# Kernel optimization log

Hardware: AMD Instinct MI355X
Metric: run time of the kernel (lower is better)

Reference implementation:

```python
import jax, jax.numpy as jnp
import numpy as np

D = 128        # embed_dims
P = 4          # num_points
G = 1          # num_groups
L = 4          # num_levels
NC = 6         # cameras
HB, WB = 200, 200
QN = HB * WB
NUM_LAYERS = 2
IMG_H, IMG_W = 256, 704
EPS = 1e-5
PC_MIN = np.array([-50.0, -50.0, -5.0], np.float32)
PC_EXT = np.array([100.0, 100.0, 8.0], np.float32)
LEVEL_HW = [(32, 88), (16, 44), (8, 22), (4, 11)]


def layer_norm(x, g, b):
    m = x.mean(-1, keepdims=True)
    v = jnp.mean((x - m) ** 2, axis=-1, keepdims=True)
    return (x - m) * jax.lax.rsqrt(v + 1e-5) * g + b


def bilinear(feat, u, v):
    # feat: (B,H,W,C); u,v: (B,N) normalized to [0,1]; zero padding, align_corners=False
    B, H, W, C = feat.shape
    x = u * W - 0.5
    y = v * H - 0.5
    x0f = jnp.floor(x)
    y0f = jnp.floor(y)
    wx = (x - x0f)[..., None]
    wy = (y - y0f)[..., None]
    x0 = x0f.astype(jnp.int32)
    y0 = y0f.astype(jnp.int32)
    bi = jnp.arange(B)[:, None]

    def gather(xi, yi):
        valid = ((xi >= 0) & (xi < W) & (yi >= 0) & (yi < H)).astype(feat.dtype)[..., None]
        return feat[bi, jnp.clip(yi, 0, H - 1), jnp.clip(xi, 0, W - 1)] * valid

    return (gather(x0, y0) * (1 - wx) * (1 - wy)
            + gather(x0 + 1, y0) * wx * (1 - wy)
            + gather(x0, y0 + 1) * (1 - wx) * wy
            + gather(x0 + 1, y0 + 1) * wx * wy)


def cam_contrib(l2i_n, hom, sw, cam_feats):
    # l2i_n: (B,4,4); hom: (B,Q,G,P,4); sw: (B,Q,G,P,L); cam_feats: L x (B,Hl,Wl,C)
    p2 = jnp.einsum('bij,bqgpj->bqgpi', l2i_n, hom)
    z = p2[..., 2]
    zc = jnp.maximum(z, EPS)
    u = p2[..., 0] / (zc * IMG_W)
    v = p2[..., 1] / (zc * IMG_H)
    mask = (z > EPS) & (u >= 0) & (u <= 1) & (v >= 0) & (v <= 1)
    B = hom.shape[0]
    uf = u.reshape(B, -1)
    vf = v.reshape(B, -1)
    out = jnp.zeros(hom.shape[:4] + (cam_feats[0].shape[-1],), cam_feats[0].dtype)
    for l in range(L):
        s = bilinear(cam_feats[l], uf, vf).reshape(B, -1, G, P, cam_feats[l].shape[-1])
        out = out + s * sw[..., l:l + 1]
    return out * mask[..., None].astype(out.dtype)


def forward(feat0, feat1, feat2, feat3, lidar2img, bev_query, bev_pos,
            pe_w1, pe_b1, pe_w2, pe_b2, conv1_w, conv1_b, conv2_w, conv2_b,
            off_w, off_b, sw_w, sw_b, cp_w1, cp_b1, cp_w2, cp_b2, cp_w3, cp_b3,
            ffn_w1, ffn_b1, ffn_w2, ffn_b2, n1_g, n1_b, n2_g, n2_b, n3_g, n3_b):
    # (b,n,C,h,w) -> (b,n,h,w,C), matching the decoder's rearrange (g=1)
    feats = [jnp.transpose(f, (0, 1, 3, 4, 2)) for f in (feat0, feat1, feat2, feat3)]
    B = bev_query.shape[0]
    pc_min = jnp.asarray(PC_MIN)
    pc_ext = jnp.asarray(PC_EXT)
    # position embedding of bev_pos is identical every layer
    pos_embed = jax.nn.relu(bev_pos @ pe_w1 + pe_b1) @ pe_w2 + pe_b2
    q = bev_query
    for _ in range(NUM_LAYERS):
        # in_conv: 1x1 conv + GELU + 5x5 conv on 200x200 BEV grid
        qe = (q + pos_embed).reshape(B, HB, WB, D)
        h = jax.nn.gelu(qe @ conv1_w + conv1_b, approximate=False)
        h = jax.lax.conv_general_dilated(h, conv2_w, (1, 1), 'SAME',
                                         dimension_numbers=('NHWC', 'HWIO', 'NHWC')) + conv2_b
        q = q + h.reshape(B, QN, D)
        q = layer_norm(q, n1_g, n1_b)
        # DetSegSampling
        off = (q @ off_w + off_b).reshape(B, QN, G, P, 3)
        ref = bev_pos[:, :, None, None, :] * pc_ext + pc_min
        pts = ref + off
        sw = jax.nn.softmax((q @ sw_w + sw_b).reshape(B, QN, G, P, L), axis=-1)
        hom = jnp.concatenate([pts, jnp.ones_like(pts[..., :1])], -1)
        acc = jnp.zeros((B, QN, G, P, D), q.dtype)
        for n in range(NC):
            acc = acc + cam_contrib(lidar2img[:, n], hom, sw,
                                    tuple(f[:, n] for f in feats))
        # 'b q g p c -> b q (p g c)' then 3-layer compressor MLP (1x1 convs)
        flat = jnp.transpose(acc, (0, 1, 3, 2, 4)).reshape(B, QN, P * G * D)
        h = jax.nn.relu(flat @ cp_w1 + cp_b1)
        h = jax.nn.relu(h @ cp_w2 + cp_b2)
        h = h @ cp_w3 + cp_b3
        q = q + h
        q = layer_norm(q, n2_g, n2_b)
        q = q + (jax.nn.relu(q @ ffn_w1 + ffn_b1) @ ffn_w2 + ffn_b2)
        q = layer_norm(q, n3_g, n3_b)
    return q


def _make_lidar2img():
    fx = fy = 500.0
    K = np.array([[fx, 0, IMG_W / 2, 0], [0, fy, IMG_H / 2, 0],
                  [0, 0, 1, 0], [0, 0, 0, 1]], np.float32)
    mats = []
    for n in range(NC):
        yaw = 2 * np.pi * n / NC
        c, s = np.cos(yaw), np.sin(yaw)
        # camera n looks along (cos yaw, sin yaw, 0), mounted 1.5m above lidar
        E = np.array([[s, -c, 0, 0], [0, 0, -1, 1.5], [c, s, 0, 0], [0, 0, 0, 1]], np.float32)
        mats.append(K @ E)
    return jnp.asarray(np.stack(mats))[None]  # (1,NC,4,4)


def setup_inputs() -> dict:
    key = jax.random.key(0)
    ks = jax.random.split(key, 24)
    sc = 0.02
    inp = {}
    for i, (h, w) in enumerate(LEVEL_HW):
        inp[f'feat{i}'] = jax.random.normal(ks[i], (1, NC, D, h, w), jnp.float32)
    inp['lidar2img'] = _make_lidar2img()
    inp['bev_query'] = jax.random.normal(ks[4], (1, QN, D), jnp.float32)
    inp['bev_pos'] = jax.random.uniform(ks[5], (1, QN, 3), jnp.float32)
    inp['pe_w1'] = jax.random.normal(ks[6], (3, 2 * D), jnp.float32) * sc
    inp['pe_b1'] = jnp.zeros((2 * D,), jnp.float32)
    inp['pe_w2'] = jax.random.normal(ks[7], (2 * D, D), jnp.float32) * sc
    inp['pe_b2'] = jnp.zeros((D,), jnp.float32)
    inp['conv1_w'] = jax.random.normal(ks[8], (D, D), jnp.float32) * sc
    inp['conv1_b'] = jnp.zeros((D,), jnp.float32)
    inp['conv2_w'] = jax.random.normal(ks[9], (5, 5, D, D), jnp.float32) * sc
    inp['conv2_b'] = jnp.zeros((D,), jnp.float32)
    inp['off_w'] = jax.random.normal(ks[10], (D, G * P * 3), jnp.float32) * 0.01
    inp['off_b'] = jax.random.uniform(ks[11], (G * P * 3,), jnp.float32, -0.5, 0.5)
    inp['sw_w'] = jax.random.normal(ks[12], (D, G * P * L), jnp.float32) * sc
    inp['sw_b'] = jnp.zeros((G * P * L,), jnp.float32)
    inp['cp_w1'] = jax.random.normal(ks[13], (P * G * D, 4 * D), jnp.float32) * sc
    inp['cp_b1'] = jnp.zeros((4 * D,), jnp.float32)
    inp['cp_w2'] = jax.random.normal(ks[14], (4 * D, 4 * D), jnp.float32) * sc
    inp['cp_b2'] = jnp.zeros((4 * D,), jnp.float32)
    inp['cp_w3'] = jax.random.normal(ks[15], (4 * D, D), jnp.float32) * sc
    inp['cp_b3'] = jnp.zeros((D,), jnp.float32)
    inp['ffn_w1'] = jax.random.normal(ks[16], (D, D), jnp.float32) * sc
    inp['ffn_b1'] = jnp.zeros((D,), jnp.float32)
    inp['ffn_w2'] = jax.random.normal(ks[17], (D, D), jnp.float32) * sc
    inp['ffn_b2'] = jnp.zeros((D,), jnp.float32)
    for i in (1, 2, 3):
        inp[f'n{i}_g'] = jnp.ones((D,), jnp.float32)
        inp[f'n{i}_b'] = jnp.zeros((D,), jnp.float32)
    return inp


def reference(feat0, feat1, feat2, feat3, lidar2img, bev_query, bev_pos,
              pe_w1, pe_b1, pe_w2, pe_b2, conv1_w, conv1_b, conv2_w, conv2_b,
              off_w, off_b, sw_w, sw_b, cp_w1, cp_b1, cp_w2, cp_b2, cp_w3, cp_b3,
              ffn_w1, ffn_b1, ffn_w2, ffn_b2, n1_g, n1_b, n2_g, n2_b, n3_g, n3_b):
    return forward(feat0, feat1, feat2, feat3, lidar2img, bev_query, bev_pos,
                   pe_w1, pe_b1, pe_w2, pe_b2, conv1_w, conv1_b, conv2_w, conv2_b,
                   off_w, off_b, sw_w, sw_b, cp_w1, cp_b1, cp_w2, cp_b2, cp_w3, cp_b3,
                   ffn_w1, ffn_b1, ffn_w2, ffn_b2, n1_g, n1_b, n2_g, n2_b, n3_g, n3_b)
```

## Files before the change

kernel.cpp:

```cpp
#include <hip/hip_runtime.h>
#include <hip/hip_bf16.h>

typedef unsigned short u16;
typedef unsigned char u8;
typedef __attribute__((ext_vector_type(8))) short bf16x8;
typedef __attribute__((ext_vector_type(4))) float f32x4;
typedef __attribute__((ext_vector_type(2))) float f32x2;

#define DEV __device__ __forceinline__

DEV float b2f(u16 s){ return __uint_as_float(((unsigned)s) << 16); }
DEV u16 f2b(float f){
    unsigned u = __float_as_uint(f);
    u = u + 0x7fffu + ((u >> 16) & 1u);
    return (u16)(u >> 16);
}
DEV u8 f2f8(float v){
    int r = __builtin_amdgcn_cvt_pk_fp8_f32(v, v, 0, false);
    return (u8)(r & 0xff);
}
DEV unsigned f2f8x4(float a, float b, float c, float d){
    int lo = __builtin_amdgcn_cvt_pk_fp8_f32(a, b, 0, false);
    int r  = __builtin_amdgcn_cvt_pk_fp8_f32(c, d, lo, true);
    return (unsigned)r;
}
DEV void storeElem(float* p, float v){ *p = v; }
DEV void storeElem(u16* p, float v){ *p = f2b(v); }
DEV void storeElem(u8* p, float v){ *p = f2f8(v); }

template<int ACT> DEV float actf(float x){
    if (ACT == 1) return fmaxf(x, 0.f);
    if (ACT == 2) return 0.5f * x * (1.f + erff(x * 0.70710678118654752f));
    return x;
}

DEV void gload16(const void* g, void* l){
    __builtin_amdgcn_global_load_lds(
        (const __attribute__((address_space(1))) void*)g,
        (__attribute__((address_space(3))) void*)l, 16, 0, 0);
}

__global__ void transpose_feat(const float* __restrict__ in, u8* __restrict__ out,
                               int H, int W){
    int total = 6 * H * W * 32;
    int lin = blockIdx.x * 256 + threadIdx.x;
    if (lin >= total) return;
    int c4   = (lin & 31) * 4;
    int pix  = lin >> 5;
    int x    = pix % W;
    int rest = pix / W;
    int y    = rest % H;
    int n    = rest / H;
    int HW   = H * W;
    size_t ib = ((size_t)(n * 128 + c4) * H + y) * W + x;
    unsigned v4 = f2f8x4(in[ib], in[ib + (size_t)HW],
                         in[ib + (size_t)2 * HW], in[ib + (size_t)3 * HW]);
    *(unsigned*)&out[(size_t)pix * 128 + c4] = v4;
}

__global__ void prep_wt(const float* __restrict__ w, u16* __restrict__ o, int K, int N){
    int id = blockIdx.x * 256 + threadIdx.x;
    if (id >= K * N) return;
    int n = id / K, k = id % K;
    o[id] = f2b(w[(size_t)k * N + n]);
}
__global__ void prep_wt_f8(const float* __restrict__ w, u8* __restrict__ o, int K, int N){
    int id = blockIdx.x * 256 + threadIdx.x;
    if (id >= K * N) return;
    int n = id / K, k = id % K;
    o[id] = f2f8(w[(size_t)k * N + n]);
}
__global__ void prep_osw_w(const float* __restrict__ off_w, const float* __restrict__ off_b,
                           const float* __restrict__ sw_w, const float* __restrict__ sw_b,
                           u16* __restrict__ owsT, float* __restrict__ obias){
    int id = blockIdx.x * 256 + threadIdx.x;
    if (id >= 4096) return;
    int n = id >> 7, k = id & 127;
    float w = (n < 12) ? off_w[k * 12 + n] : (n < 28) ? sw_w[k * 16 + (n - 12)] : 0.f;
    owsT[n * 128 + k] = f2b(w);
    if (k == 0) obias[n] = (n < 12) ? off_b[n] : (n < 28) ? sw_b[n - 12] : 0.f;
}
__global__ void prep_conv_w_f8(const float* __restrict__ w, u8* __restrict__ o){
    int id = blockIdx.x * 256 + threadIdx.x;
    if (id >= 51200) return;
    int slot = id & 15;
    int oc   = (id >> 4) & 127;
    int tap  = id >> 11;
    int ks = slot >> 2, kg = slot & 3;
    int ic0 = ks * 32 + kg * 8;
    u8 tmp[8];
#pragma unroll
    for (int j = 0; j < 8; j++)
        tmp[j] = f2f8(w[((size_t)tap * 128 + ic0 + j) * 128 + oc]);
    *(long*)&o[(size_t)tap * 16384 + ks * 4096 + kg * 1024 + oc * 8] = *(long*)tmp;
}
__global__ void prep_hid(const float* __restrict__ bev_pos,
                         const float* __restrict__ w1, const float* __restrict__ b1,
                         u16* __restrict__ hid){
    int id = blockIdx.x * 256 + threadIdx.x;
    if (id >= 2560000) return;
    int qi = id >> 6, c4 = (id & 63) * 4;
    float p0 = bev_pos[qi * 3 + 0];
    float p1 = bev_pos[qi * 3 + 1];
    float p2 = bev_pos[qi * 3 + 2];
    ushort4 v;
    u16* vp = (u16*)&v;
#pragma unroll
    for (int j = 0; j < 4; j++){
        int ch = c4 + j;
        float h = p0 * w1[ch] + p1 * w1[256 + ch] + p2 * w1[512 + ch] + b1[ch];
        vp[j] = f2b(fmaxf(h, 0.f));
    }
    *(ushort4*)&hid[(size_t)qi * 256 + c4] = v;
}

DEV void stage64(const u16* __restrict__ g, int ldk, u16* lds, int wv, int lane){
    const u16* gp = g + (size_t)(lane >> 3) * ldk + (lane & 7) * 8;
#pragma unroll
    for (int j = 0; j < 4; j++){
        int ch = wv + j * 4;
        gload16(gp + (size_t)ch * 8 * ldk, lds + ch * 512);
    }
}
DEV void stage64f8(const u8* __restrict__ g, int ldk, u8* lds, int wv, int lane){
    int rloc = lane >> 2;
#pragma unroll
    for (int j = 0; j < 2; j++){
        int ch = wv + j * 4;
        int row = ch * 16 + rloc;
        int sp  = (lane & 3) ^ ((row >> 1) & 3);
        gload16(g + (size_t)row * ldk + sp * 16, lds + ch * 1024);
    }
}

template<int K, int ACT, typename TOUT, int NBY = 0, int NBX = 0>
__global__ __launch_bounds__(256) void mfma_gemm(
    const u16* __restrict__ A, const u16* __restrict__ BT,
    const float* __restrict__ bias, TOUT* __restrict__ C, int Ntot){
    __shared__ u16 As[2][128 * 64];
    __shared__ u16 Bs[2][128 * 64];
    const int t = threadIdx.x, wv = t >> 6, lane = t & 63;
    int bx, by;
    if (NBY > 0){
        const int gpx = (NBX + 7) / 8;
        int xcd = blockIdx.x & 7, slot = blockIdx.x >> 3;
        bx = xcd * gpx + slot / NBY;
        by = slot % NBY;
        if (bx >= NBX) return;
    } else { bx = blockIdx.x; by = blockIdx.y; }
    const int r0 = bx * 128, n0 = by * 128;
    const int l15 = lane & 15, kg = lane >> 4;
    const int wr = (wv >> 1) * 64, wc = (wv & 1) * 64;
    f32x4 acc[4][4];
#pragma unroll
    for (int r = 0; r < 4; r++)
#pragma unroll
        for (int c = 0; c < 4; c++) acc[r][c] = (f32x4){0.f, 0.f, 0.f, 0.f};

    stage64(A + (size_t)r0 * K, K, As[0], wv, lane);
    stage64(BT + (size_t)n0 * K, K, Bs[0], wv, lane);
    __syncthreads();
    int buf = 0;
    for (int kc = 0; kc < K / 64; kc++){
        if (kc + 1 < K / 64){
            stage64(A + (size_t)r0 * K + (kc + 1) * 64, K, As[buf ^ 1], wv, lane);
            stage64(BT + (size_t)n0 * K + (kc + 1) * 64, K, Bs[buf ^ 1], wv, lane);
        }
#pragma unroll
        for (int ks = 0; ks < 2; ks++){
            bf16x8 af[4], bfr[4];
#pragma unroll
            for (int r = 0; r < 4; r++)
                af[r] = *(const bf16x8*)&As[buf][(wr + r * 16 + l15) * 64 + ks * 32 + kg * 8];
#pragma unroll
            for (int c = 0; c < 4; c++)
                bfr[c] = *(const bf16x8*)&Bs[buf][(wc + c * 16 + l15) * 64 + ks * 32 + kg * 8];
#pragma unroll
            for (int r = 0; r < 4; r++)
#pragma unroll
                for (int c = 0; c < 4; c++)
                    acc[r][c] = __builtin_amdgcn_mfma_f32_16x16x32_bf16(af[r], bfr[c], acc[r][c], 0, 0, 0);
        }
        __syncthreads();
        buf ^= 1;
    }
#pragma unroll
    for (int c = 0; c < 4; c++){
        int gcol = n0 + wc + c * 16 + l15;
        float bb = bias[gcol];
#pragma unroll
        for (int r = 0; r < 4; r++){
#pragma unroll
            for (int reg = 0; reg < 4; reg++){
                int grow = r0 + wr + r * 16 + kg * 4 + reg;
                storeElem(C + (size_t)grow * Ntot + gcol, actf<ACT>(acc[r][c][reg] + bb));
            }
        }
    }
}

template<int K, int ACT, typename TOUT, int NBY = 0, int NBX = 0>
__global__ __launch_bounds__(256) void mfma_gemm_f8(
    const u8* __restrict__ A, const u8* __restrict__ BT,
    const float* __restrict__ bias, TOUT* __restrict__ C, int Ntot){
    __shared__ __align__(16) u8 As[2][128 * 64];
    __shared__ __align__(16) u8 Bs[2][128 * 64];
    const int t = threadIdx.x, wv = t >> 6, lane = t & 63;
    int bx, by;
    if (NBY > 0){
        const int gpx = (NBX + 7) / 8;
        int xcd = blockIdx.x & 7, slot = blockIdx.x >> 3;
        bx = xcd * gpx + slot / NBY;
        by = slot % NBY;
        if (bx >= NBX) return;
    } else { bx = blockIdx.x; by = blockIdx.y; }
    const int r0 = bx * 128, n0 = by * 128;
    const int l15 = lane & 15, kg = lane >> 4;
    const int wr = (wv >> 1) * 64, wc = (wv & 1) * 64;
    f32x4 acc[4][4];
#pragma unroll
    for (int r = 0; r < 4; r++)
#pragma unroll
        for (int c = 0; c < 4; c++) acc[r][c] = (f32x4){0.f, 0.f, 0.f, 0.f};

    stage64f8(A + (size_t)r0 * K, K, As[0], wv, lane);
    stage64f8(BT + (size_t)n0 * K, K, Bs[0], wv, lane);
    __syncthreads();
    int buf = 0;
    for (int kc = 0; kc < K / 64; kc++){
        if (kc + 1 < K / 64){
            stage64f8(A + (size_t)r0 * K + (kc + 1) * 64, K, As[buf ^ 1], wv, lane);
            stage64f8(BT + (size_t)n0 * K + (kc + 1) * 64, K, Bs[buf ^ 1], wv, lane);
        }
#pragma unroll
        for (int ks = 0; ks < 2; ks++){
            long af[4], bfr[4];
#pragma unroll
            for (int r = 0; r < 4; r++){
                int row = wr + r * 16 + l15;
                int s8 = (ks * 4 + kg) ^ (row & 6);
                af[r] = *(const long*)&As[buf][row * 64 + s8 * 8];
            }
#pragma unroll
            for (int c = 0; c < 4; c++){
                int row = wc + c * 16 + l15;
                int s8 = (ks * 4 + kg) ^ (row & 6);
                bfr[c] = *(const long*)&Bs[buf][row * 64 + s8 * 8];
            }
#pragma unroll
            for (int r = 0; r < 4; r++)
#pragma unroll
                for (int c = 0; c < 4; c++)
                    acc[r][c] = __builtin_amdgcn_mfma_f32_16x16x32_fp8_fp8(af[r], bfr[c], acc[r][c], 0, 0, 0);
        }
        __syncthreads();
        buf ^= 1;
    }
#pragma unroll
    for (int c = 0; c < 4; c++){
        int gcol = n0 + wc + c * 16 + l15;
        float bb = bias[gcol];
#pragma unroll
        for (int r = 0; r < 4; r++){
#pragma unroll
            for (int reg = 0; reg < 4; reg++){
                int grow = r0 + wr + r * 16 + kg * 4 + reg;
                storeElem(C + (size_t)grow * Ntot + gcol, actf<ACT>(acc[r][c][reg] + bb));
            }
        }
    }
}

__global__ __launch_bounds__(256) void mfma_pos(
    const u16* __restrict__ A, const u16* __restrict__ BT,
    const float* __restrict__ bias, const float* __restrict__ bq,
    float* __restrict__ pos, u16* __restrict__ qp16){
    const int K = 256;
    __shared__ u16 As[2][128 * 64];
    __shared__ u16 Bs[2][128 * 64];
    const int t = threadIdx.x, wv = t >> 6, lane = t & 63;
    const int r0 = blockIdx.x * 128;
    const int l15 = lane & 15, kg = lane >> 4;
    const int wr = (wv >> 1) * 64, wc = (wv & 1) * 64;
    f32x4 acc[4][4];
#pragma unroll
    for (int r = 0; r < 4; r++)
#pragma unroll
        for (int c = 0; c < 4; c++) acc[r][c] = (f32x4){0.f, 0.f, 0.f, 0.f};

    stage64(A + (size_t)r0 * K, K, As[0], wv, lane);
    stage64(BT, K, Bs[0], wv, lane);
    __syncthreads();
    int buf = 0;
    for (int kc = 0; kc < 4; kc++){
        if (kc + 1 < 4){
            stage64(A + (size_t)r0 * K + (kc + 1) * 64, K, As[buf ^ 1], wv, lane);
            stage64(BT + (kc + 1) * 64, K, Bs[buf ^ 1], wv, lane);
        }
#pragma unroll
        for (int ks = 0; ks < 2; ks++){
            bf16x8 af[4], bfr[4];
#pragma unroll
            for (int r = 0; r < 4; r++)
                af[r] = *(const bf16x8*)&As[buf][(wr + r * 16 + l15) * 64 + ks * 32 + kg * 8];
#pragma unroll
            for (int c = 0; c < 4; c++)
                bfr[c] = *(const bf16x8*)&Bs[buf][(wc + c * 16 + l15) * 64 + ks * 32 + kg * 8];
#pragma unroll
            for (int r = 0; r < 4; r++)
#pragma unroll
                for (int c = 0; c < 4; c++)
                    acc[r][c] = __builtin_amdgcn_mfma_f32_16x16x32_bf16(af[r], bfr[c], acc[r][c], 0, 0, 0);
        }
        __syncthreads();
        buf ^= 1;
    }
#pragma unroll
    for (int c = 0; c < 4; c++){
        int gcol = wc + c * 16 + l15;
        float bb = bias[gcol];
#pragma unroll
        for (int r = 0; r < 4; r++){
#pragma unroll
            for (int reg = 0; reg < 4; reg++){
                int grow = r0 + wr + r * 16 + kg * 4 + reg;
                int growc = min(grow, 39999);
                float v = acc[r][c][reg] + bb;
                pos[(size_t)grow * 128 + gcol]  = v;
                qp16[(size_t)grow * 128 + gcol] = f2b(v + bq[(size_t)growc * 128 + gcol]);
            }
        }
    }
}

template<int AUXM>
__global__ __launch_bounds__(256) void mfma_ffn_ln(
    const u16* __restrict__ A, const u16* __restrict__ W1T,
    const float* __restrict__ b1, const u16* __restrict__ W2T,
    const float* __restrict__ b2, const float* __restrict__ qin,
    const float* __restrict__ gam, const float* __restrict__ bet,
    float* __restrict__ outf, u16* __restrict__ aux,
    const float* __restrict__ pos, int Mlim){
    __shared__ u16 As[2][128 * 64];
    __shared__ u16 Bs[2][128 * 64];
    const int t = threadIdx.x, wv = t >> 6, lane = t & 63;
    const int r0 = blockIdx.x * 128;
    const int l15 = lane & 15, kg = lane >> 4;
    const int wr = wv * 32;
    f32x4 acc[2][8];
#pragma unroll
    for (int r = 0; r < 2; r++)
#pragma unroll
        for (int c = 0; c < 8; c++) acc[r][c] = (f32x4){0.f, 0.f, 0.f, 0.f};

    stage64(A + (size_t)r0 * 128, 128, As[0], wv, lane);
    stage64(A + (size_t)r0 * 128 + 64, 128, As[1], wv, lane);
    stage64(W1T, 128, Bs[0], wv, lane);
    stage64(W1T + 64, 128, Bs[1], wv, lane);
    __syncthreads();
#pragma unroll
    for (int kc = 0; kc < 2; kc++){
#pragma unroll
        for (int ks = 0; ks < 2; ks++){
            bf16x8 af[2], bfr[8];
#pragma unroll
            for (int r = 0; r < 2; r++)
                af[r] = *(const bf16x8*)&As[kc][(wr + r * 16 + l15) * 64 + ks * 32 + kg * 8];
#pragma unroll
            for (int c = 0; c < 8; c++)
                bfr[c] = *(const bf16x8*)&Bs[kc][(c * 16 + l15) * 64 + ks * 32 + kg * 8];
#pragma unroll
            for (int r = 0; r < 2; r++)
#pragma unroll
                for (int c = 0; c < 8; c++)
                    acc[r][c] = __builtin_amdgcn_mfma_f32_16x16x32_bf16(af[r], bfr[c], acc[r][c], 0, 0, 0);
        }
    }
    __syncthreads();
    stage64(W2T, 128, Bs[0], wv, lane);
    stage64(W2T + 64, 128, Bs[1], wv, lane);
#pragma unroll
    for (int c = 0; c < 8; c++){
        int col = c * 16 + l15;
        float bb1 = b1[col];
#pragma unroll
        for (int r = 0; r < 2; r++)
#pragma unroll
            for (int reg = 0; reg < 4; reg++){
                int rowl = wr + r * 16 + kg * 4 + reg;
                As[col >> 6][rowl * 64 + (col & 63)] = f2b(fmaxf(acc[r][c][reg] + bb1, 0.f));
            }
    }
    __syncthreads();
#pragma unroll
    for (int r = 0; r < 2; r++)
#pragma unroll
        for (int c = 0; c < 8; c++) acc[r][c] = (f32x4){0.f, 0.f, 0.f, 0.f};
#pragma unroll
    for (int kc = 0; kc < 2; kc++){
#pragma unroll
        for (int ks = 0; ks < 2; ks++){
            bf16x8 af[2], bfr[8];
#pragma unroll
            for (int r = 0; r < 2; r++)
                af[r] = *(const bf16x8*)&As[kc][(wr + r * 16 + l15) * 64 + ks * 32 + kg * 8];
#pragma unroll
            for (int c = 0; c < 8; c++)
                bfr[c] = *(const bf16x8*)&Bs[kc][(c * 16 + l15) * 64 + ks * 32 + kg * 8];
#pragma unroll
            for (int r = 0; r < 2; r++)
#pragma unroll
                for (int c = 0; c < 8; c++)
                    acc[r][c] = __builtin_amdgcn_mfma_f32_16x16x32_bf16(af[r], bfr[c], acc[r][c], 0, 0, 0);
        }
    }
    float bb[8], gg[8], be[8];
#pragma unroll
    for (int c = 0; c < 8; c++){
        int col = c * 16 + l15;
        bb[c] = b2[col]; gg[c] = gam[col]; be[c] = bet[col];
    }
#pragma unroll
    for (int r = 0; r < 2; r++){
#pragma unroll
        for (int reg = 0; reg < 4; reg++){
            int grow = r0 + wr + r * 16 + kg * 4 + reg;
            const float* qrow = qin + (size_t)grow * 128;
            float s = 0.f, q2 = 0.f;
#pragma unroll
            for (int c = 0; c < 8; c++){
                float x = acc[r][c][reg] + bb[c] + qrow[c * 16 + l15];
                acc[r][c][reg] = x;
                s += x; q2 += x * x;
            }
#pragma unroll
            for (int m = 8; m >= 1; m >>= 1){
                s  += __shfl_xor(s, m, 64);
                q2 += __shfl_xor(q2, m, 64);
            }
            float mean = s * 0.0078125f;
            float var  = q2 * 0.0078125f - mean * mean;
            float rs   = rsqrtf(var + 1e-5f);
            bool wr_ok = grow < Mlim;
#pragma unroll
            for (int c = 0; c < 8; c++){
                float o = (acc[r][c][reg] - mean) * rs * gg[c] + be[c];
                int col = c * 16 + l15;
                if (wr_ok){
                    outf[(size_t)grow * 128 + col] = o;
                    if (AUXM == 2)
                        aux[(size_t)grow * 128 + col] = f2b(o + pos[(size_t)grow * 128 + col]);
                }
            }
        }
    }
}

template<int K, int AUXM>
__global__ __launch_bounds__(256) void mfma_gemm_ln_f8(
    const u8* __restrict__ A, const u8* __restrict__ BT,
    const float* __restrict__ bias, const float* __restrict__ qin,
    const float* __restrict__ gam, const float* __restrict__ bet,
    float* __restrict__ outf, u16* __restrict__ aux,
    const float* __restrict__ pos, int Mlim){
    __shared__ __align__(16) u8 As[2][128 * 64];
    __shared__ __align__(16) u8 Bs[2][128 * 64];
    const int t = threadIdx.x, wv = t >> 6, lane = t & 63;
    const int r0 = blockIdx.x * 128;
    const int l15 = lane & 15, kg = lane >> 4;
    const int wr = wv * 32;
    f32x4 acc[2][8];
#pragma unroll
    for (int r = 0; r < 2; r++)
#pragma unroll
        for (int c = 0; c < 8; c++) acc[r][c] = (f32x4){0.f, 0.f, 0.f, 0.f};

    stage64f8(A + (size_t)r0 * K, K, As[0], wv, lane);
    stage64f8(BT, K, Bs[0], wv, lane);
    __syncthreads();
    int buf = 0;
    for (int kc = 0; kc < K / 64; kc++){
        if (kc + 1 < K / 64){
            stage64f8(A + (size_t)r0 * K + (kc + 1) * 64, K, As[buf ^ 1], wv, lane);
            stage64f8(BT + (kc + 1) * 64, K, Bs[buf ^ 1], wv, lane);
        }
#pragma unroll
        for (int ks = 0; ks < 2; ks++){
            long af[2], bfr[8];
#pragma unroll
            for (int r = 0; r < 2; r++){
                int row = wr + r * 16 + l15;
                int s8 = (ks * 4 + kg) ^ (row & 6);
                af[r] = *(const long*)&As[buf][row * 64 + s8 * 8];
            }
#pragma unroll
            for (int c = 0; c < 8; c++){
                int row = c * 16 + l15;
                int s8 = (ks * 4 + kg) ^ (row & 6);
                bfr[c] = *(const long*)&Bs[buf][row * 64 + s8 * 8];
            }
#pragma unroll
            for (int r = 0; r < 2; r++)
#pragma unroll
                for (int c = 0; c < 8; c++)
                    acc[r][c] = __builtin_amdgcn_mfma_f32_16x16x32_fp8_fp8(af[r], bfr[c], acc[r][c], 0, 0, 0);
        }
        __syncthreads();
        buf ^= 1;
    }
    float bb[8], gg[8], be[8];
#pragma unroll
    for (int c = 0; c < 8; c++){
        int col = c * 16 + l15;
        bb[c] = bias[col]; gg[c] = gam[col]; be[c] = bet[col];
    }
#pragma unroll
    for (int r = 0; r < 2; r++){
#pragma unroll
        for (int reg = 0; reg < 4; reg++){
            int grow = r0 + wr + r * 16 + kg * 4 + reg;
            const float* qrow = qin + (size_t)grow * 128;
            float s = 0.f, q2 = 0.f;
#pragma unroll
            for (int c = 0; c < 8; c++){
                float x = acc[r][c][reg] + bb[c] + qrow[c * 16 + l15];
                acc[r][c][reg] = x;
                s += x; q2 += x * x;
            }
#pragma unroll
            for (int m = 8; m >= 1; m >>= 1){
                s  += __shfl_xor(s, m, 64);
                q2 += __shfl_xor(q2, m, 64);
            }
            float mean = s * 0.0078125f;
            float var  = q2 * 0.0078125f - mean * mean;
            float rs   = rsqrtf(var + 1e-5f);
            bool wr_ok = grow < Mlim;
#pragma unroll
            for (int c = 0; c < 8; c++){
                float o = (acc[r][c][reg] - mean) * rs * gg[c] + be[c];
                int col = c * 16 + l15;
                if (wr_ok){
                    outf[(size_t)grow * 128 + col] = o;
                    if (AUXM == 1) aux[(size_t)grow * 128 + col] = f2b(o);
                    else if (AUXM == 2)
                        aux[(size_t)grow * 128 + col] = f2b(o + pos[(size_t)grow * 128 + col]);
                }
            }
        }
    }
}

__global__ __launch_bounds__(256) void mfma_osw(
    const u16* __restrict__ A, const u16* __restrict__ BT,
    const float* __restrict__ bias, float* __restrict__ osw){
    __shared__ u16 As[2][128 * 64];
    __shared__ u16 Bs[2][32 * 64];
    const int t = threadIdx.x, wv = t >> 6, lane = t & 63;
    const int r0 = blockIdx.x * 128;
    const int l15 = lane & 15, kg = lane >> 4;
#pragma unroll
    for (int it = 0; it < 8; it++){
        int id = it * 256 + t;
        int row = id >> 4, slot = id & 15;
        uint4 v = *(const uint4*)&A[(size_t)(r0 + row) * 128 + slot * 8];
        *(uint4*)&As[slot >> 3][row * 64 + (slot & 7) * 8] = v;
    }
#pragma unroll
    for (int it = 0; it < 2; it++){
        int id = it * 256 + t;
        if (id < 512){
            int row = id >> 4, slot = id & 15;
            uint4 v = *(const uint4*)&BT[(size_t)row * 128 + slot * 8];
            *(uint4*)&Bs[slot >> 3][row * 64 + (slot & 7) * 8] = v;
        }
    }
    __syncthreads();
    f32x4 acc[2][2];
#pragma unroll
    for (int r = 0; r < 2; r++)
#pragma unroll
        for (int c = 0; c < 2; c++) acc[r][c] = (f32x4){0.f, 0.f, 0.f, 0.f};
#pragma unroll
    for (int ks = 0; ks < 4; ks++){
        int h = ks >> 1, koff = (ks & 1) * 32 + kg * 8;
        bf16x8 af[2], bfr[2];
#pragma unroll
        for (int r = 0; r < 2; r++)
            af[r] = *(const bf16x8*)&As[h][(wv * 32 + r * 16 + l15) * 64 + koff];
#pragma unroll
        for (int c = 0; c < 2; c++)
            bfr[c] = *(const bf16x8*)&Bs[h][(c * 16 + l15) * 64 + koff];
#pragma unroll
        for (int r = 0; r < 2; r++)
#pragma unroll
            for (int c = 0; c < 2; c++)
                acc[r][c] = __builtin_amdgcn_mfma_f32_16x16x32_bf16(af[r], bfr[c], acc[r][c], 0, 0, 0);
    }
#pragma unroll
    for (int c = 0; c < 2; c++){
        int gcol = c * 16 + l15;
        float bb = bias[gcol];
#pragma unroll
        for (int r = 0; r < 2; r++)
#pragma unroll
            for (int reg = 0; reg < 4; reg++){
                int grow = r0 + wv * 32 + r * 16 + kg * 4 + reg;
                osw[(size_t)grow * 32 + gcol] = acc[r][c][reg] + bb;
            }
    }
}

__global__ __launch_bounds__(256) void proj_kernel(
    const float* __restrict__ osw, const float* __restrict__ bev_pos,
    const float* __restrict__ l2i, float* __restrict__ ent, int* __restrict__ cntb){
    int id = blockIdx.x * 256 + threadIdx.x;
    int qi = id >> 2, p = id & 3;
    const float* row = osw + (size_t)qi * 32;
    float px = bev_pos[qi * 3 + 0] * 100.f - 50.f + row[p * 3 + 0];
    float py = bev_pos[qi * 3 + 1] * 100.f - 50.f + row[p * 3 + 1];
    float pz = bev_pos[qi * 3 + 2] * 8.f   - 5.f  + row[p * 3 + 2];
    float lg[4];
#pragma unroll
    for (int l = 0; l < 4; l++) lg[l] = row[12 + p * 4 + l];
    float mx = fmaxf(fmaxf(lg[0], lg[1]), fmaxf(lg[2], lg[3]));
    float den = 0.f, sw[4];
#pragma unroll
    for (int l = 0; l < 4; l++){ sw[l] = expf(lg[l] - mx); den += sw[l]; }
    float inv = 1.f / den;
#pragma unroll
    for (int l = 0; l < 4; l++) sw[l] *= inv;

    const int HS[4] = {32, 16, 8, 4};
    const int WS[4] = {88, 44, 22, 11};
    const unsigned LOFF[4] = {0u, 2162688u, 2703360u, 2838528u};
    int cnt = 0;
    for (int cam = 0; cam < 6; cam++){
        const float* M = l2i + cam * 16;
        float t0 = M[0] * px + M[1] * py + M[2]  * pz + M[3];
        float t1 = M[4] * px + M[5] * py + M[6]  * pz + M[7];
        float z  = M[8] * px + M[9] * py + M[10] * pz + M[11];
        float zc = fmaxf(z, 1e-5f);
        float u = t0 / (zc * 704.f);
        float v = t1 / (zc * 256.f);
        if (!((z > 1e-5f) && u >= 0.f && u <= 1.f && v >= 0.f && v <= 1.f)) continue;
#pragma unroll
        for (int l = 0; l < 4; l++){
            const int Hl = HS[l], Wl = WS[l];
            float xx = u * (float)Wl - 0.5f;
            float yy = v * (float)Hl - 0.5f;
            float xf = floorf(xx), yf = floorf(yy);
            float wx = xx - xf, wy = yy - yf;
            int ix = (int)xf, iy = (int)yf;
            float sl = sw[l];
            float wx0 = (ix >= 0)      ? 1.f - wx : 0.f;
            float wx1 = (ix < Wl - 1)  ? wx       : 0.f;
            float wy0 = (iy >= 0)      ? 1.f - wy : 0.f;
            float wy1 = (iy < Hl - 1)  ? wy       : 0.f;
            int x0c = max(ix, 0), x1c = min(ix + 1, Wl - 1);
            int y0c = max(iy, 0), y1c = min(iy + 1, Hl - 1);
            unsigned base = LOFF[l] + (unsigned)cam * (unsigned)(Hl * Wl * 128)
                          + (unsigned)(y0c * Wl + x0c) * 128u;
            unsigned dxdy = (unsigned)((x1c - x0c) * 128)
                          | ((unsigned)((y1c - y0c) * Wl * 128) << 16);
            if (cnt < 8){
                float* ep = ent + ((size_t)cnt * 160000 + id) * 8;
                float4 w4;
                w4.x = sl * wx0 * wy0; w4.y = sl * wx1 * wy0;
                w4.z = sl * wx0 * wy1; w4.w = sl * wx1 * wy1;
                *(float4*)ep = w4;
                float4 m4;
                m4.x = __uint_as_float(base); m4.y = __uint_as_float(dxdy);
                m4.z = 0.f; m4.w = 0.f;
                *(float4*)(ep + 4) = m4;
                cnt++;
            }
        }
    }
    cntb[id] = cnt;
}

DEV void fma8f8(float* acc, uint2 v, float w){
    f32x2 p0 = __builtin_amdgcn_cvt_pk_f32_fp8(v.x, false);
    f32x2 p1 = __builtin_amdgcn_cvt_pk_f32_fp8(v.x, true);
    f32x2 p2 = __builtin_amdgcn_cvt_pk_f32_fp8(v.y, false);
    f32x2 p3 = __builtin_amdgcn_cvt_pk_f32_fp8(v.y, true);
    acc[0] = fmaf(p0.x, w, acc[0]);
    acc[1] = fmaf(p0.y, w, acc[1]);
    acc[2] = fmaf(p1.x, w, acc[2]);
    acc[3] = fmaf(p1.y, w, acc[3]);
    acc[4] = fmaf(p2.x, w, acc[4]);
    acc[5] = fmaf(p2.y, w, acc[5]);
    acc[6] = fmaf(p3.x, w, acc[6]);
    acc[7] = fmaf(p3.y, w, acc[7]);
}

__global__ __launch_bounds__(256) void sample_kernel(
    const float* __restrict__ ent, const int* __restrict__ cntb,
    const u8* __restrict__ ftbase, u8* __restrict__ flat){
    const int t = threadIdx.x;
    const int lane = t & 15;
    const int id = blockIdx.x * 16 + (t >> 4);
    const int d0 = lane * 8;
    const int cnt = cntb[id];
    float acc[8] = {0, 0, 0, 0, 0, 0, 0, 0};

    float4 wA, wB; float2 mA, mB;
    if (cnt > 0){
        const float* ep = ent + ((size_t)id) * 8;
        wA = *(const float4*)ep;
        mA = *(const float2*)(ep + 4);
    }
    for (int e = 0; e < cnt; e++){
        if (e + 1 < cnt){
            const float* ep = ent + ((size_t)(e + 1) * 160000 + id) * 8;
            wB = *(const float4*)ep;
            mB = *(const float2*)(ep + 4);
        }
        unsigned base = __float_as_uint(mA.x) + (unsigned)d0;
        unsigned dxdy = __float_as_uint(mA.y);
        unsigned dx = dxdy & 0xffffu, dy = dxdy >> 16;
        uint2 v00 = *(const uint2*)(ftbase + base);
        uint2 v10 = *(const uint2*)(ftbase + base + dx);
        uint2 v01 = *(const uint2*)(ftbase + base + dy);
        uint2 v11 = *(const uint2*)(ftbase + base + dx + dy);
        fma8f8(acc, v00, wA.x);
        fma8f8(acc, v10, wA.y);
        fma8f8(acc, v01, wA.z);
        fma8f8(acc, v11, wA.w);
        wA = wB; mA = mB;
    }
    uint2 o;
    o.x = f2f8x4(acc[0], acc[1], acc[2], acc[3]);
    o.y = f2f8x4(acc[4], acc[5], acc[6], acc[7]);
    *(uint2*)&flat[(size_t)id * 128 + d0] = o;
}

#define ALOAD(S, DST) if ((S) < 100){                                                 \
    const int tap_ = (S) >> 2, ks_ = (S) & 3;                                         \
    const int ky_ = tap_ / 5, kx_ = tap_ - ky_ * 5;                                   \
    const int s8_ = ks_ * 4 + kg;                                                     \
    _Pragma("unroll")                                                                 \
    for (int fb = 0; fb < 2; fb++){                                                   \
        _Pragma("unroll")                                                             \
        for (int fp = 0; fp < 2; fp++){                                               \
            int pr_ = fb * 4 + (l15 >> 2) + ky_;                                      \
            int pc_ = fp * 4 + (l15 & 3) + kx_;                                       \
            int pix_ = pr_ * 12 + pc_;                                                \
            int sw_ = ((s8_ >> 1) ^ (pc_ + 4 * pr_)) & 7;                             \
            DST[fb * 2 + fp] = *(const long*)((const char*)Ps + pix_ * 128            \
                                              + sw_ * 16 + (s8_ & 1) * 8);            \
        }                                                                             \
    }                                                                                 \
}
#define CMFMA(CURA, CURB) {                                                           \
    _Pragma("unroll")                                                                 \
    for (int fr = 0; fr < 4; fr++){                                                   \
        acc[fr][0] = __builtin_amdgcn_mfma_f32_16x16x32_fp8_fp8(CURA[fr], CURB[0], acc[fr][0], 0, 0, 0); \
        acc[fr][1] = __builtin_amdgcn_mfma_f32_16x16x32_fp8_fp8(CURA[fr], CURB[1], acc[fr][1], 0, 0, 0); \
    }                                                                                 \
}
#define LOADB(S, DST) if ((S) < 100){                                                 \
    const u8* wp_ = wfrag + ((S) >> 2) * 16384 + ((S) & 3) * 4096                     \
                   + kg * 1024 + (wc + l15) * 8;                                      \
    DST[0] = *(const long*)(wp_);                                                     \
    DST[1] = *(const long*)(wp_ + 128);                                               \
}

__global__ __launch_bounds__(256, 4) void conv5_ln(
    const u8* __restrict__ in,
    const u8* __restrict__ wfrag,
    const float* __restrict__ bias,
    const float* __restrict__ qin,
    const float* __restrict__ gam, const float* __restrict__ bet,
    float* __restrict__ qb, u16* __restrict__ q16){
    __shared__ __align__(16) u8 Ps[144 * 128];
    const int t = threadIdx.x, wv = t >> 6, lane = t & 63;
    const int bx = blockIdx.x % 25, by = blockIdx.x / 25;
    const int x0 = bx * 8, y0 = by * 8;
    const int l15 = lane & 15, kg = lane >> 4;
    const int wc = wv * 32;

#pragma unroll
    for (int it = 0; it < 5; it++){
        int id = it * 256 + t;
        if (id < 1152){
            int pix = id >> 3, slot = id & 7;
            int pr = pix / 12, pc = pix - pr * 12;
            int gy = y0 + pr - 2, gx = x0 + pc - 2;
            uint4 v = {0u, 0u, 0u, 0u};
            if (gy >= 0 && gy < 200 && gx >= 0 && gx < 200)
                v = *(const uint4*)&in[(size_t)(gy * 200 + gx) * 128 + slot * 16];
            int s = (slot ^ (pc + 4 * pr)) & 7;
            *(uint4*)((char*)Ps + pix * 128 + s * 16) = v;
        }
    }
    f32x4 acc[4][2];
#pragma unroll
    for (int r = 0; r < 4; r++){
        acc[r][0] = (f32x4){0.f, 0.f, 0.f, 0.f};
        acc[r][1] = (f32x4){0.f, 0.f, 0.f, 0.f};
    }

    long b0[2], b1[2], b2[2], b3[2];
    LOADB(0, b0); LOADB(1, b1); LOADB(2, b2);
    __syncthreads();

    long aA[4], aB[4];
    ALOAD(0, aA);

    for (int i = 0; i < 25; i++){
        int s = i * 4;
        LOADB(s + 3, b3); ALOAD(s + 1, aB); CMFMA(aA, b0);
        LOADB(s + 4, b0); ALOAD(s + 2, aA); CMFMA(aB, b1);
        LOADB(s + 5, b1); ALOAD(s + 3, aB); CMFMA(aA, b2);
        LOADB(s + 6, b2); ALOAD(s + 4, aA); CMFMA(aB, b3);
    }
    __syncthreads();

    float* part = (float*)Ps;
    float bb[2], gg[2], be[2];
#pragma unroll
    for (int c = 0; c < 2; c++){
        int oc = wc + c * 16 + l15;
        bb[c] = bias[oc]; gg[c] = gam[oc]; be[c] = bet[oc];
    }
#pragma unroll
    for (int fb = 0; fb < 2; fb++){
#pragma unroll
        for (int fp = 0; fp < 2; fp++){
#pragma unroll
            for (int reg = 0; reg < 4; reg++){
                int py = fb * 4 + kg, px = fp * 4 + reg;
                int lp = py * 8 + px;
                int grow = (y0 + py) * 200 + x0 + px;
                const float* qrow = qin + (size_t)grow * 128;
                float s = 0.f, q2 = 0.f;
#pragma unroll
                for (int c = 0; c < 2; c++){
                    float x = acc[fb * 2 + fp][c][reg] + bb[c] + qrow[wc + c * 16 + l15];
                    acc[fb * 2 + fp][c][reg] = x;
                    s += x; q2 += x * x;
                }
#pragma unroll
                for (int msk = 8; msk >= 1; msk >>= 1){
                    s  += __shfl_xor(s, msk, 64);
                    q2 += __shfl_xor(q2, msk, 64);
                }
                if (l15 == 0){
                    part[lp * 8 + wv * 2 + 0] = s;
                    part[lp * 8 + wv * 2 + 1] = q2;
                }
            }
        }
    }
    __syncthreads();
#pragma unroll
    for (int fb = 0; fb < 2; fb++){
#pragma unroll
        for (int fp = 0; fp < 2; fp++){
#pragma unroll
            for (int reg = 0; reg < 4; reg++){
                int py = fb * 4 + kg, px = fp * 4 + reg;
                int lp = py * 8 + px;
                int grow = (y0 + py) * 200 + x0 + px;
                float s  = part[lp * 8 + 0] + part[lp * 8 + 2] + part[lp * 8 + 4] + part[lp * 8 + 6];
                float q2 = part[lp * 8 + 1] + part[lp * 8 + 3] + part[lp * 8 + 5] + part[lp * 8 + 7];
                float mean = s * 0.0078125f;
                float var  = q2 * 0.0078125f - mean * mean;
                float rs   = rsqrtf(var + 1e-5f);
#pragma unroll
                for (int c = 0; c < 2; c++){
                    int oc = wc + c * 16 + l15;
                    float o = (acc[fb * 2 + fp][c][reg] - mean) * rs * gg[c] + be[c];
                    qb[(size_t)grow * 128 + oc]  = o;
                    q16[(size_t)grow * 128 + oc] = f2b(o);
                }
            }
        }
    }
}

extern "C" void kernel_launch(void* const* d_in, const int* in_sizes, int n_in,
                              void* d_out, int out_size, void* d_ws, size_t ws_size,
                              hipStream_t stream){
    const float* feat0   = (const float*)d_in[0];
    const float* feat1   = (const float*)d_in[1];
    const float* feat2   = (const float*)d_in[2];
    const float* feat3   = (const float*)d_in[3];
    const float* l2i     = (const float*)d_in[4];
    const float* bev_q   = (const float*)d_in[5];
    const float* bev_pos = (const float*)d_in[6];
    const float* pe_w1   = (const float*)d_in[7];
    const float* pe_b1   = (const float*)d_in[8];
    const float* pe_w2   = (const float*)d_in[9];
    const float* pe_b2   = (const float*)d_in[10];
    const float* conv1_w = (const float*)d_in[11];
    const float* conv1_b = (const float*)d_in[12];
    const float* conv2_w = (const float*)d_in[13];
    const float* conv2_b = (const float*)d_in[14];
    const float* off_w   = (const float*)d_in[15];
    const float* off_b   = (const float*)d_in[16];
    const float* sw_w    = (const float*)d_in[17];
    const float* sw_b    = (const float*)d_in[18];
    const float* cp_w1   = (const float*)d_in[19];
    const float* cp_b1   = (const float*)d_in[20];
    const float* cp_w2   = (const float*)d_in[21];
    const float* cp_b2   = (const float*)d_in[22];
    const float* cp_w3   = (const float*)d_in[23];
    const float* cp_b3   = (const float*)d_in[24];
    const float* ffn_w1  = (const float*)d_in[25];
    const float* ffn_b1  = (const float*)d_in[26];
    const float* ffn_w2  = (const float*)d_in[27];
    const float* ffn_b2  = (const float*)d_in[28];
    const float* n1g = (const float*)d_in[29];
    const float* n1b = (const float*)d_in[30];
    const float* n2g = (const float*)d_in[31];
    const float* n2b = (const float*)d_in[32];
    const float* n3g = (const float*)d_in[33];
    const float* n3b = (const float*)d_in[34];

    float* base   = (float*)d_ws;
    float* pos    = base;
    float* qb     = base + 5128192;
    float* hbuf   = base + 10256384;
    u8*    h18    = (u8*)hbuf;
    float* ent    = hbuf;
    u16*   q16    = (u16*)(base + 20512768);
    u16*   qpos16 = (u16*)(base + 23076864);
    int*   cntb   = (int*)qpos16;
    u8*    bufA8  = (u8*)(base + 25640960);
    float* osw    = (float*)(base + 25640960 + 1310720);
    u8*    flat8  = (u8*)(base + 28205056);
    u16*   hid16  = (u16*)flat8;
    u8*    ft0    = (u8*)(base + 38461440);
    u8*    ft1    = ft0 + 6 * 32 * 88 * 128;
    u8*    ft2    = ft1 + 6 * 16 * 44 * 128;
    u8*    ft3    = ft2 + 6 * 8 * 22 * 128;
    u8*    w1t8   = (u8*)(base + 39897600);
    u8*    w2t8   = w1t8 + 512 * 512;
    u8*    w3t8   = w2t8 + 512 * 512;
    u16*   wc1t   = (u16*)(base + 40192512);
    u16*   wf1t   = (u16*)(base + 40200704);
    u16*   wf2t   = (u16*)(base + 40208896);
    u16*   owsT   = (u16*)(base + 40217088);
    float* obias  = (float*)(base + 40219136);
    u8*    wcs8   = (u8*)(base + 40219168);
    u16*   pw2t   = (u16*)(base + 40424168);
    float* outp   = (float*)d_out;

    transpose_feat<<<(6 * 32 * 88 * 32 + 255) / 256, 256, 0, stream>>>(feat0, ft0, 32, 88);
    transpose_feat<<<(6 * 16 * 44 * 32 + 255) / 256, 256, 0, stream>>>(feat1, ft1, 16, 44);
    transpose_feat<<<(6 * 8 * 22 * 32 + 255) / 256, 256, 0, stream>>>(feat2, ft2, 8, 22);
    transpose_feat<<<(6 * 4 * 11 * 32 + 255) / 256, 256, 0, stream>>>(feat3, ft3, 4, 11);
    prep_wt_f8<<<(512 * 512 + 255) / 256, 256, 0, stream>>>(cp_w1, w1t8, 512, 512);
    prep_wt_f8<<<(512 * 512 + 255) / 256, 256, 0, stream>>>(cp_w2, w2t8, 512, 512);
    prep_wt_f8<<<(512 * 128 + 255) / 256, 256, 0, stream>>>(cp_w3, w3t8, 512, 128);
    prep_wt<<<(128 * 128 + 255) / 256, 256, 0, stream>>>(conv1_w, wc1t, 128, 128);
    prep_wt<<<(128 * 128 + 255) / 256, 256, 0, stream>>>(ffn_w1, wf1t, 128, 128);
    prep_wt<<<(128 * 128 + 255) / 256, 256, 0, stream>>>(ffn_w2, wf2t, 128, 128);
    prep_wt<<<(256 * 128 + 255) / 256, 256, 0, stream>>>(pe_w2, pw2t, 256, 128);
    prep_osw_w<<<16, 256, 0, stream>>>(off_w, off_b, sw_w, sw_b, owsT, obias);
    prep_conv_w_f8<<<(51200 + 255) / 256, 256, 0, stream>>>(conv2_w, wcs8);
    prep_hid<<<10000, 256, 0, stream>>>(bev_pos, pe_w1, pe_b1, hid16);
    mfma_pos<<<313, 256, 0, stream>>>(hid16, pw2t, pe_b2, bev_q, pos, qpos16);

    for (int layer = 0; layer < 2; layer++){
        const float* qin = layer ? qb : bev_q;
        mfma_gemm<128, 2, u8><<<dim3(313, 1), 256, 0, stream>>>(qpos16, wc1t, conv1_b, bufA8, 128);
        conv5_ln<<<625, 256, 0, stream>>>(bufA8, wcs8, conv2_b, qin, n1g, n1b, qb, q16);
        mfma_osw<<<313, 256, 0, stream>>>(q16, owsT, obias, osw);
        proj_kernel<<<625, 256, 0, stream>>>(osw, bev_pos, l2i, ent, cntb);
        sample_kernel<<<10000, 256, 0, stream>>>(ent, cntb, ft0, flat8);
        mfma_gemm_f8<512, 1, u8, 4, 313><<<1280, 256, 0, stream>>>(flat8, w1t8, cp_b1, h18, 512);
        mfma_gemm_f8<512, 1, u8, 4, 313><<<1280, 256, 0, stream>>>(h18, w2t8, cp_b2, flat8, 512);
        mfma_gemm_ln_f8<512, 1><<<313, 256, 0, stream>>>(flat8, w3t8, cp_b3, qb, n2g, n2b,
                                                         qb, q16, nullptr, 40064);
        if (layer == 0)
            mfma_ffn_ln<2><<<313, 256, 0, stream>>>(q16, wf1t, ffn_b1, wf2t, ffn_b2,
                                                    qb, n3g, n3b, qb, qpos16, pos, 40064);
        else
            mfma_ffn_ln<0><<<313, 256, 0, stream>>>(q16, wf1t, ffn_b1, wf2t, ffn_b2,
                                                    qb, n3g, n3b, outp, nullptr, nullptr, 40000);
    }
}
```

Before: 436.6 us.

## Carry residual query stream in bf16 and pack sampling entries to 16 bytes

Drops the fp32 residual query buffer. Each LN kernel now reads the residual from the bf16 q16 buffer and writes only bf16, and bev_query is converted to bf16 once at the start. Projection entries shrink from 32 to 16 bytes by storing the bilinear weights as bf16 pairs. Both changes cut global memory traffic across several kernels, at the cost of bf16 rounding in the residual path and in the sampling weights. Several kernels now read and write q16 in place, which is safe only if each block's tile stays self-contained (conv5 reads a neighbourhood from bufA8, not q16).

```diff
diff --git a/kernel.cpp b/kernel.cpp
--- a/kernel.cpp
+++ b/kernel.cpp
@@ -69,6 +69,13 @@
     if (id >= K * N) return;
     int n = id / K, k = id % K;
     o[id] = f2f8(w[(size_t)k * N + n]);
+}
+__global__ void prep_cvt16(const float* __restrict__ src, u16* __restrict__ dst, int n4){
+    int i4 = blockIdx.x * 256 + threadIdx.x;
+    if (i4 >= n4) return;
+    float4 a = *(const float4*)&src[(size_t)i4 * 4];
+    ushort4 v; v.x = f2b(a.x); v.y = f2b(a.y); v.z = f2b(a.z); v.w = f2b(a.w);
+    *(ushort4*)&dst[(size_t)i4 * 4] = v;
 }
 __global__ void prep_osw_w(const float* __restrict__ off_w, const float* __restrict__ off_b,
                            const float* __restrict__ sw_w, const float* __restrict__ sw_b,
@@ -337,9 +344,9 @@
 __global__ __launch_bounds__(256) void mfma_ffn_ln(
     const u16* __restrict__ A, const u16* __restrict__ W1T,
     const float* __restrict__ b1, const u16* __restrict__ W2T,
-    const float* __restrict__ b2, const float* __restrict__ qin,
+    const float* __restrict__ b2, const u16* __restrict__ qin16,
     const float* __restrict__ gam, const float* __restrict__ bet,
-    float* __restrict__ outf, u16* __restrict__ aux,
+    float* __restrict__ outf, u16* __restrict__ q16out, u16* __restrict__ auxpos,
     const float* __restrict__ pos, int Mlim){
     __shared__ u16 As[2][128 * 64];
     __shared__ u16 Bs[2][128 * 64];
@@ -425,11 +432,11 @@
 #pragma unroll
         for (int reg = 0; reg < 4; reg++){
             int grow = r0 + wr + r * 16 + kg * 4 + reg;
-            const float* qrow = qin + (size_t)grow * 128;
+            const u16* qrow = qin16 + (size_t)grow * 128;
             float s = 0.f, q2 = 0.f;
 #pragma unroll
             for (int c = 0; c < 8; c++){
-                float x = acc[r][c][reg] + bb[c] + qrow[c * 16 + l15];
+                float x = acc[r][c][reg] + bb[c] + b2f(qrow[c * 16 + l15]);
                 acc[r][c][reg] = x;
                 s += x; q2 += x * x;
             }
@@ -447,22 +454,24 @@
                 float o = (acc[r][c][reg] - mean) * rs * gg[c] + be[c];
                 int col = c * 16 + l15;
                 if (wr_ok){
-                    outf[(size_t)grow * 128 + col] = o;
-                    if (AUXM == 2)
-                        aux[(size_t)grow * 128 + col] = f2b(o + pos[(size_t)grow * 128 + col]);
+                    if (AUXM == 0){
+                        outf[(size_t)grow * 128 + col] = o;
+                    } else {
+                        q16out[(size_t)grow * 128 + col] = f2b(o);
+                        auxpos[(size_t)grow * 128 + col] = f2b(o + pos[(size_t)grow * 128 + col]);
+                    }
                 }
             }
         }
     }
 }
 
-template<int K, int AUXM>
+template<int K>
 __global__ __launch_bounds__(256) void mfma_gemm_ln_f8(
     const u8* __restrict__ A, const u8* __restrict__ BT,
-    const float* __restrict__ bias, const float* __restrict__ qin,
+    const float* __restrict__ bias, const u16* __restrict__ qin16,
     const float* __restrict__ gam, const float* __restrict__ bet,
-    float* __restrict__ outf, u16* __restrict__ aux,
-    const float* __restrict__ pos, int Mlim){
+    u16* __restrict__ q16out, int Mlim){
     __shared__ __align__(16) u8 As[2][128 * 64];
     __shared__ __align__(16) u8 Bs[2][128 * 64];
     const int t = threadIdx.x, wv = t >> 6, lane = t & 63;
@@ -519,11 +528,11 @@
 #pragma unroll
         for (int reg = 0; reg < 4; reg++){
             int grow = r0 + wr + r * 16 + kg * 4 + reg;
-            const float* qrow = qin + (size_t)grow * 128;
+            const u16* qrow = qin16 + (size_t)grow * 128;
             float s = 0.f, q2 = 0.f;
 #pragma unroll
             for (int c = 0; c < 8; c++){
-                float x = acc[r][c][reg] + bb[c] + qrow[c * 16 + l15];
+                float x = acc[r][c][reg] + bb[c] + b2f(qrow[c * 16 + l15]);
                 acc[r][c][reg] = x;
                 s += x; q2 += x * x;
             }
@@ -539,13 +548,7 @@
 #pragma unroll
             for (int c = 0; c < 8; c++){
                 float o = (acc[r][c][reg] - mean) * rs * gg[c] + be[c];
-                int col = c * 16 + l15;
-                if (wr_ok){
-                    outf[(size_t)grow * 128 + col] = o;
-                    if (AUXM == 1) aux[(size_t)grow * 128 + col] = f2b(o);
-                    else if (AUXM == 2)
-                        aux[(size_t)grow * 128 + col] = f2b(o + pos[(size_t)grow * 128 + col]);
-                }
+                if (wr_ok) q16out[(size_t)grow * 128 + c * 16 + l15] = f2b(o);
             }
         }
     }
@@ -613,7 +616,7 @@
 
 __global__ __launch_bounds__(256) void proj_kernel(
     const float* __restrict__ osw, const float* __restrict__ bev_pos,
-    const float* __restrict__ l2i, float* __restrict__ ent, int* __restrict__ cntb){
+    const float* __restrict__ l2i, uint4* __restrict__ ent4, int* __restrict__ cntb){
     int id = blockIdx.x * 256 + threadIdx.x;
     int qi = id >> 2, p = id & 3;
     const float* row = osw + (size_t)qi * 32;
@@ -664,15 +667,12 @@
             unsigned dxdy = (unsigned)((x1c - x0c) * 128)
                           | ((unsigned)((y1c - y0c) * Wl * 128) << 16);
             if (cnt < 8){
-                float* ep = ent + ((size_t)cnt * 160000 + id) * 8;
-                float4 w4;
-                w4.x = sl * wx0 * wy0; w4.y = sl * wx1 * wy0;
-                w4.z = sl * wx0 * wy1; w4.w = sl * wx1 * wy1;
-                *(float4*)ep = w4;
-                float4 m4;
-                m4.x = __uint_as_float(base); m4.y = __uint_as_float(dxdy);
-                m4.z = 0.f; m4.w = 0.f;
-                *(float4*)(ep + 4) = m4;
+                uint4 e4;
+                e4.x = (unsigned)f2b(sl * wx0 * wy0) | ((unsigned)f2b(sl * wx1 * wy0) << 16);
+                e4.y = (unsigned)f2b(sl * wx0 * wy1) | ((unsigned)f2b(sl * wx1 * wy1) << 16);
+                e4.z = base;
+                e4.w = dxdy;
+                ent4[(size_t)cnt * 160000 + id] = e4;
                 cnt++;
             }
         }
@@ -696,7 +696,7 @@
 }
 
 __global__ __launch_bounds__(256) void sample_kernel(
-    const float* __restrict__ ent, const int* __restrict__ cntb,
+    const uint4* __restrict__ ent4, const int* __restrict__ cntb,
     const u8* __restrict__ ftbase, u8* __restrict__ flat){
     const int t = threadIdx.x;
     const int lane = t & 15;
@@ -705,30 +705,21 @@
     const int cnt = cntb[id];
     float acc[8] = {0, 0, 0, 0, 0, 0, 0, 0};
 
-    float4 wA, wB; float2 mA, mB;
-    if (cnt > 0){
-        const float* ep = ent + ((size_t)id) * 8;
-        wA = *(const float4*)ep;
-        mA = *(const float2*)(ep + 4);
-    }
+    uint4 evA, evB;
+    if (cnt > 0) evA = ent4[(size_t)id];
     for (int e = 0; e < cnt; e++){
-        if (e + 1 < cnt){
-            const float* ep = ent + ((size_t)(e + 1) * 160000 + id) * 8;
-            wB = *(const float4*)ep;
-            mB = *(const float2*)(ep + 4);
-        }
-        unsigned base = __float_as_uint(mA.x) + (unsigned)d0;
-        unsigned dxdy = __float_as_uint(mA.y);
-        unsigned dx = dxdy & 0xffffu, dy = dxdy >> 16;
+        if (e + 1 < cnt) evB = ent4[(size_t)(e + 1) * 160000 + id];
+        unsigned base = evA.z + (unsigned)d0;
+        unsigned dx = evA.w & 0xffffu, dy = evA.w >> 16;
         uint2 v00 = *(const uint2*)(ftbase + base);
         uint2 v10 = *(const uint2*)(ftbase + base + dx);
         uint2 v01 = *(const uint2*)(ftbase + base + dy);
         uint2 v11 = *(const uint2*)(ftbase + base + dx + dy);
-        fma8f8(acc, v00, wA.x);
-        fma8f8(acc, v10, wA.y);
-        fma8f8(acc, v01, wA.z);
-        fma8f8(acc, v11, wA.w);
-        wA = wB; mA = mB;
+        fma8f8(acc, v00, b2f((u16)(evA.x & 0xffffu)));
+        fma8f8(acc, v10, b2f((u16)(evA.x >> 16)));
+        fma8f8(acc, v01, b2f((u16)(evA.y & 0xffffu)));
+        fma8f8(acc, v11, b2f((u16)(evA.y >> 16)));
+        evA = evB;
     }
     uint2 o;
     o.x = f2f8x4(acc[0], acc[1], acc[2], acc[3]);
@@ -771,9 +762,9 @@
     const u8* __restrict__ in,
     const u8* __restrict__ wfrag,
     const float* __restrict__ bias,
-    const float* __restrict__ qin,
+    const u16* __restrict__ qin16,
     const float* __restrict__ gam, const float* __restrict__ bet,
-    float* __restrict__ qb, u16* __restrict__ q16){
+    u16* __restrict__ q16){
     __shared__ __align__(16) u8 Ps[144 * 128];
     const int t = threadIdx.x, wv = t >> 6, lane = t & 63;
     const int bx = blockIdx.x % 25, by = blockIdx.x / 25;
@@ -834,11 +825,11 @@
                 int py = fb * 4 + kg, px = fp * 4 + reg;
                 int lp = py * 8 + px;
                 int grow = (y0 + py) * 200 + x0 + px;
-                const float* qrow = qin + (size_t)grow * 128;
+                const u16* qrow = qin16 + (size_t)grow * 128;
                 float s = 0.f, q2 = 0.f;
 #pragma unroll
                 for (int c = 0; c < 2; c++){
-                    float x = acc[fb * 2 + fp][c][reg] + bb[c] + qrow[wc + c * 16 + l15];
+                    float x = acc[fb * 2 + fp][c][reg] + bb[c] + b2f(qrow[wc + c * 16 + l15]);
                     acc[fb * 2 + fp][c][reg] = x;
                     s += x; q2 += x * x;
                 }
@@ -873,7 +864,6 @@
                 for (int c = 0; c < 2; c++){
                     int oc = wc + c * 16 + l15;
                     float o = (acc[fb * 2 + fp][c][reg] - mean) * rs * gg[c] + be[c];
-                    qb[(size_t)grow * 128 + oc]  = o;
                     q16[(size_t)grow * 128 + oc] = f2b(o);
                 }
             }
@@ -922,10 +912,10 @@
 
     float* base   = (float*)d_ws;
     float* pos    = base;
-    float* qb     = base + 5128192;
+    u16*   bq16   = (u16*)(base + 5128192);
     float* hbuf   = base + 10256384;
     u8*    h18    = (u8*)hbuf;
-    float* ent    = hbuf;
+    uint4* ent4   = (uint4*)hbuf;
     u16*   q16    = (u16*)(base + 20512768);
     u16*   qpos16 = (u16*)(base + 23076864);
     int*   cntb   = (int*)qpos16;
@@ -962,25 +952,26 @@
     prep_wt<<<(256 * 128 + 255) / 256, 256, 0, stream>>>(pe_w2, pw2t, 256, 128);
     prep_osw_w<<<16, 256, 0, stream>>>(off_w, off_b, sw_w, sw_b, owsT, obias);
     prep_conv_w_f8<<<(51200 + 255) / 256, 256, 0, stream>>>(conv2_w, wcs8);
+    prep_cvt16<<<5000, 256, 0, stream>>>(bev_q, bq16, 1280000);
     prep_hid<<<10000, 256, 0, stream>>>(bev_pos, pe_w1, pe_b1, hid16);
     mfma_pos<<<313, 256, 0, stream>>>(hid16, pw2t, pe_b2, bev_q, pos, qpos16);
 
     for (int layer = 0; layer < 2; layer++){
-        const float* qin = layer ? qb : bev_q;
+        const u16* qin16 = layer ? q16 : bq16;
         mfma_gemm<128, 2, u8><<<dim3(313, 1), 256, 0, stream>>>(qpos16, wc1t, conv1_b, bufA8, 128);
-        conv5_ln<<<625, 256, 0, stream>>>(bufA8, wcs8, conv2_b, qin, n1g, n1b, qb, q16);
+        conv5_ln<<<625, 256, 0, stream>>>(bufA8, wcs8, conv2_b, qin16, n1g, n1b, q16);
         mfma_osw<<<313, 256, 0, stream>>>(q16, owsT, obias, osw);
-        proj_kernel<<<625, 256, 0, stream>>>(osw, bev_pos, l2i, ent, cntb);
-        sample_kernel<<<10000, 256, 0, stream>>>(ent, cntb, ft0, flat8);
+        proj_kernel<<<625, 256, 0, stream>>>(osw, bev_pos, l2i, ent4, cntb);
+        sample_kernel<<<10000, 256, 0, stream>>>(ent4, cntb, ft0, flat8);
         mfma_gemm_f8<512, 1, u8, 4, 313><<<1280, 256, 0, stream>>>(flat8, w1t8, cp_b1, h18, 512);
         mfma_gemm_f8<512, 1, u8, 4, 313><<<1280, 256, 0, stream>>>(h18, w2t8, cp_b2, flat8, 512);
-        mfma_gemm_ln_f8<512, 1><<<313, 256, 0, stream>>>(flat8, w3t8, cp_b3, qb, n2g, n2b,
-                                                         qb, q16, nullptr, 40064);
+        mfma_gemm_ln_f8<512><<<313, 256, 0, stream>>>(flat8, w3t8, cp_b3, q16, n2g, n2b,
+                                                      q16, 40064);
         if (layer == 0)
             mfma_ffn_ln<2><<<313, 256, 0, stream>>>(q16, wf1t, ffn_b1, wf2t, ffn_b2,
-                                                    qb, n3g, n3b, qb, qpos16, pos, 40064);
+                                                    q16, n3g, n3b, nullptr, q16, qpos16, pos, 40064);
         else
             mfma_ffn_ln<0><<<313, 256, 0, stream>>>(q16, wf1t, ffn_b1, wf2t, ffn_b2,
-                                                    qb, n3g, n3b, outp, nullptr, nullptr, 40000);
-    }
-}
+                                                    q16, n3g, n3b, outp, nullptr, nullptr, nullptr, 40000);
+    }
+}
```

Measured after the change: 422.6 us. 3.2% less time.
